# Optimization experiments

Measured on AMD Instinct MI355X. Metric: run time of the kernel, lower is better.

## Reference

```python
import jax, jax.numpy as jnp
import numpy as np

N_NODES = 50000
N_EDGES = 800000
D = 128        # in_channels == out_channels
EDGE_DIM = 32
EPS = 0.0      # GINEConv default eps


def setup_inputs() -> dict:
    key = jax.random.key(0)
    ks = jax.random.split(key, 12)
    s = lambda d: 1.0 / np.sqrt(d)
    inp = {
        "x": jax.random.normal(ks[0], (N_NODES, D), jnp.float32),
        "edge_index": jax.random.randint(ks[1], (2, N_EDGES), 0, N_NODES, jnp.int64),
        "edge_attr": jax.random.normal(ks[2], (N_EDGES, EDGE_DIM), jnp.float32),
        "importance": jax.random.uniform(ks[3], (N_NODES, 1), jnp.float32),
        # GINEConv edge lin: Linear(edge_dim, in_channels)
        "We": jax.random.uniform(ks[4], (EDGE_DIM, D), jnp.float32, -s(EDGE_DIM), s(EDGE_DIM)),
        "be": jax.random.uniform(ks[5], (D,), jnp.float32, -s(EDGE_DIM), s(EDGE_DIM)),
        # GINEConv nn: Linear(in_channels, out_channels)
        "Wc": jax.random.uniform(ks[6], (D, D), jnp.float32, -s(D), s(D)),
        "bc": jax.random.uniform(ks[7], (D,), jnp.float32, -s(D), s(D)),
        # importance_gate: Linear(out_channels + 1, out_channels)
        "Wg": jax.random.uniform(ks[8], (D + 1, D), jnp.float32, -s(D + 1), s(D + 1)),
        "bg": jax.random.uniform(ks[9], (D,), jnp.float32, -s(D + 1), s(D + 1)),
        # importance_propagation: Linear(out_channels, 1)
        "Wp": jax.random.uniform(ks[10], (D, 1), jnp.float32, -s(D), s(D)),
        "bp": jax.random.uniform(ks[11], (1,), jnp.float32, -s(D), s(D)),
    }
    return inp


def reference(x, edge_index, edge_attr, importance, We, be, Wc, bc, Wg, bg, Wp, bp):
    src, dst = edge_index[0], edge_index[1]
    # GINEConv: messages = relu(x_j + lin(edge_attr)), aggregated by sum at dst
    e = edge_attr @ We + be                      # [E, D]
    msg = jax.nn.relu(x[src] + e)                # [E, D] gather + fused add/relu
    agg = jax.ops.segment_sum(msg, dst, num_segments=N_NODES)  # [N, D] scatter-add
    conv_out = ((1.0 + EPS) * x + agg) @ Wc + bc  # [N, D]
    # importance gating + residual
    gate_in = jnp.concatenate([conv_out, importance], axis=-1)  # [N, D+1]
    gate = jax.nn.sigmoid(gate_in @ Wg + bg)
    out = gate * conv_out + (1.0 - gate) * x
    propagated_importance = out @ Wp + bp        # [N, 1]
    return (out, propagated_importance)
```

## Files before the change

### kernel.cpp

```cpp
#include <hip/hip_runtime.h>

#define NN 50000
#define NE 800000
#define DD 128
#define ED 32
#define NB 196

typedef short  bf16x8 __attribute__((ext_vector_type(8)));
typedef float  f32x4  __attribute__((ext_vector_type(4)));
typedef float  f32x16 __attribute__((ext_vector_type(16)));

__device__ __forceinline__ float4 ld4(const float* p) {
    return *reinterpret_cast<const float4*>(p);
}
__device__ __forceinline__ short f2bf(float f) {
    unsigned u = __float_as_uint(f);
    u += 0x7fffu + ((u >> 16) & 1u);
    return (short)(u >> 16);
}
__device__ __forceinline__ float bf2f(short h) {
    return __uint_as_float(((unsigned)(unsigned short)h) << 16);
}
__device__ __forceinline__ int sniff64(const int* ei) {
    return ((ei[1] | ei[3] | ei[5] | ei[7]) == 0) ? 1 : 0;
}

__global__ __launch_bounds__(256)
void k_setup(const float* __restrict__ x, const int* __restrict__ ei,
             const float* __restrict__ We, unsigned int* __restrict__ xb,
             int* __restrict__ counts, unsigned short* __restrict__ Bft)
{
    const int tid = threadIdx.x;
    if (blockIdx.x < 6250) {
        const int t = blockIdx.x * 256 + tid;
        if (t >= NN * 32) return;
        const int n = t >> 5, c = t & 31;
        const float* xr = x + (size_t)n * DD + c;
        const unsigned b0 = (unsigned short)f2bf(xr[0]);
        const unsigned b1 = (unsigned short)f2bf(xr[32]);
        const unsigned b2 = (unsigned short)f2bf(xr[64]);
        const unsigned b3 = (unsigned short)f2bf(xr[96]);
        xb[(size_t)n * 64 + c * 2]     = b0 | (b1 << 16);
        xb[(size_t)n * 64 + c * 2 + 1] = b2 | (b3 << 16);
    } else if (blockIdx.x < 8298) {
        const int is64 = sniff64(ei);
        const int2* ei2 = (const int2*)ei;
        for (int e = (blockIdx.x - 6250) * 256 + tid; e < NE; e += 2048 * 256) {
            const int dst = is64 ? ei2[NE + e].x : ei[NE + e];
            atomicAdd(&counts[dst], 1);
        }
    } else if (tid < 64) {
        const int col = tid & 31, h = tid >> 5;
#pragma unroll
        for (int bb = 0; bb < 4; ++bb)
#pragma unroll
            for (int s = 0; s < 2; ++s)
#pragma unroll
                for (int i = 0; i < 8; ++i)
                    Bft[tid * 64 + (bb * 2 + s) * 8 + i] =
                        (unsigned short)f2bf(We[(s * 16 + h * 8 + i) * DD + bb * 32 + col]);
    }
}

__global__ __launch_bounds__(256)
void k_bsum(const int* __restrict__ counts, int* __restrict__ bsum) {
    const int i = blockIdx.x * 256 + threadIdx.x;
    int c = (i < NN) ? counts[i] : 0;
#pragma unroll
    for (int off = 32; off; off >>= 1) c += __shfl_xor(c, off, 64);
    __shared__ int ws4[4];
    if ((threadIdx.x & 63) == 0) ws4[threadIdx.x >> 6] = c;
    __syncthreads();
    if (threadIdx.x == 0) bsum[blockIdx.x] = ws4[0] + ws4[1] + ws4[2] + ws4[3];
}

__global__ __launch_bounds__(256)
void k_scanb(const int* __restrict__ bsum, int* __restrict__ bexcl) {
    const int tid = threadIdx.x, lane = tid & 63, w = tid >> 6;
    const int v = (tid < NB) ? bsum[tid] : 0;
    int s = v;
#pragma unroll
    for (int off = 1; off < 64; off <<= 1) {
        const int t = __shfl_up(s, off, 64);
        if (lane >= off) s += t;
    }
    __shared__ int wsum[4], wexcl[4];
    if (lane == 63) wsum[w] = s;
    __syncthreads();
    if (tid == 0) {
        int r = 0;
#pragma unroll
        for (int k = 0; k < 4; ++k) { wexcl[k] = r; r += wsum[k]; }
    }
    __syncthreads();
    if (tid < NB) bexcl[tid] = wexcl[w] + s - v;
}

__global__ __launch_bounds__(256)
void k_rowptr(const int* __restrict__ counts, const int* __restrict__ bexcl,
              int* __restrict__ cursor) {
    const int tid = threadIdx.x, lane = tid & 63, w = tid >> 6;
    const int i = blockIdx.x * 256 + tid;
    const int c = (i < NN) ? counts[i] : 0;
    int s = c;
#pragma unroll
    for (int off = 1; off < 64; off <<= 1) {
        const int t = __shfl_up(s, off, 64);
        if (lane >= off) s += t;
    }
    __shared__ int wsum[4], wexcl[4];
    if (lane == 63) wsum[w] = s;
    __syncthreads();
    if (tid == 0) {
        int r = 0;
#pragma unroll
        for (int k = 0; k < 4; ++k) { wexcl[k] = r; r += wsum[k]; }
    }
    __syncthreads();
    if (i < NN) cursor[i] = bexcl[blockIdx.x] + wexcl[w] + s - c;
}

__global__ __launch_bounds__(256)
void k_scatter2(const int* __restrict__ ei, int* __restrict__ cursor,
                const float* __restrict__ ea, int* __restrict__ sdat4,
                unsigned int* __restrict__ ebs)
{
    const int tid = threadIdx.x;
    const int e0  = blockIdx.x * 128;
    __shared__ int spos[128];
    if (tid < 128) {
        const int is64 = sniff64(ei);
        const int2* ei2 = (const int2*)ei;
        const int e   = e0 + tid;
        const int src = is64 ? ei2[e].x : ei[e];
        const int dst = is64 ? ei2[NE + e].x : ei[NE + e];
        const int pos = atomicAdd(&cursor[dst], 1);
        sdat4[pos] = src | (dst << 16);
        spos[tid] = pos;
    }
    __syncthreads();
#pragma unroll
    for (int it = 0; it < 8; ++it) {
        const int task = it * 256 + tid;
        const int el   = task >> 4;
        const int part = task & 15;
        const float2 v = *reinterpret_cast<const float2*>(
                             ea + (size_t)(e0 + el) * ED + part * 2);
        const unsigned lo = (unsigned short)f2bf(v.x);
        const unsigned hi = (unsigned short)f2bf(v.y);
        ebs[(size_t)spos[el] * 16 + part] = lo | (hi << 16);
    }
}

__device__ __forceinline__ void agg_epilogue(f32x16 (&C)[4], const float beb[4],
                                             int dstv, int lane, int col, int h,
                                             float* __restrict__ agg)
{
#pragma unroll
    for (int bb = 0; bb < 4; ++bb)
#pragma unroll
        for (int reg = 0; reg < 16; ++reg)
            C[bb][reg] = fmaxf(C[bb][reg] + beb[bb], 0.0f);

    const int  prv  = __shfl(dstv, (lane == 0) ? 0 : lane - 1, 64);
    const bool flag = (lane < 32) && ((col == 0) || (dstv != prv));
    unsigned rem = (unsigned)(__ballot(flag) & 0xFFFFFFFFull);

    while (rem) {
        const int ms = __ffs((int)rem) - 1;
        rem &= rem - 1;
        const int hi = rem ? (__ffs((int)rem) - 1) : 32;
        const int d  = __shfl(dstv, ms, 64);

        float v0 = 0.f, v1 = 0.f, v2 = 0.f, v3 = 0.f;
#pragma unroll
        for (int reg = 0; reg < 16; ++reg) {
            const int E = (reg & 3) + 8 * (reg >> 2) + 4 * h;
            const float mk = (E >= ms && E < hi) ? 1.0f : 0.0f;
            v0 = fmaf(mk, C[0][reg], v0);
            v1 = fmaf(mk, C[1][reg], v1);
            v2 = fmaf(mk, C[2][reg], v2);
            v3 = fmaf(mk, C[3][reg], v3);
        }
        v0 += __shfl_xor(v0, 32, 64);
        v1 += __shfl_xor(v1, 32, 64);
        v2 += __shfl_xor(v2, 32, 64);
        v3 += __shfl_xor(v3, 32, 64);

        float* ar = agg + (size_t)d * DD + h * 64 + col;
        unsafeAtomicAdd(ar,      h ? v2 : v0);
        unsafeAtomicAdd(ar + 32, h ? v3 : v1);
    }
}

__global__ __launch_bounds__(256, 2)
void k_aggE(const unsigned int* __restrict__ xb, const unsigned int* __restrict__ ebs,
            const unsigned short* __restrict__ Bft, const float* __restrict__ be,
            const int* __restrict__ sdat4, float* __restrict__ agg)
{
    const int lane = threadIdx.x & 63;
    const int col  = lane & 31;
    const int h    = lane >> 5;
    const int wid  = (blockIdx.x << 2) | (threadIdx.x >> 6);
    const int c0   = wid * 2, c1 = wid * 2 + 1;

    bf16x8 Bf[4][2];
    {
        const bf16x8* bp_ = reinterpret_cast<const bf16x8*>(Bft + lane * 64);
#pragma unroll
        for (int bb = 0; bb < 4; ++bb) {
            Bf[bb][0] = bp_[bb * 2];
            Bf[bb][1] = bp_[bb * 2 + 1];
        }
    }
    float beb[4];
#pragma unroll
    for (int bb = 0; bb < 4; ++bb) beb[bb] = be[bb * 32 + col];

    const int sd0 = sdat4[c0 * 32 + col];
    const int sd1 = sdat4[c1 * 32 + col];
    const unsigned int* ebr0 = ebs + ((size_t)c0 * 32 + col) * 16;
    const unsigned int* ebr1 = ebs + ((size_t)c1 * 32 + col) * 16;
    const bf16x8 A00 = *reinterpret_cast<const bf16x8*>(ebr0 + h * 4);
    const bf16x8 A01 = *reinterpret_cast<const bf16x8*>(ebr0 + 8 + h * 4);
    const bf16x8 A10 = *reinterpret_cast<const bf16x8*>(ebr1 + h * 4);
    const bf16x8 A11 = *reinterpret_cast<const bf16x8*>(ebr1 + 8 + h * 4);

    uint2 w0[16];
#pragma unroll
    for (int reg = 0; reg < 16; ++reg) {
        const int E   = (reg & 3) + 8 * (reg >> 2) + 4 * h;
        const int src = __shfl(sd0, E, 64) & 0xFFFF;
        w0[reg] = *reinterpret_cast<const uint2*>(xb + (size_t)src * 64 + col * 2);
    }

    f32x16 C[4];
#pragma unroll
    for (int reg = 0; reg < 16; ++reg) {
        C[0][reg] = __uint_as_float(w0[reg].x << 16);
        C[1][reg] = __uint_as_float(w0[reg].x & 0xFFFF0000u);
        C[2][reg] = __uint_as_float(w0[reg].y << 16);
        C[3][reg] = __uint_as_float(w0[reg].y & 0xFFFF0000u);
    }
#pragma unroll
    for (int bb = 0; bb < 4; ++bb) {
        C[bb] = __builtin_amdgcn_mfma_f32_32x32x16_bf16(A00, Bf[bb][0], C[bb], 0, 0, 0);
        C[bb] = __builtin_amdgcn_mfma_f32_32x32x16_bf16(A01, Bf[bb][1], C[bb], 0, 0, 0);
    }

    uint2 w1[16];
#pragma unroll
    for (int reg = 0; reg < 16; ++reg) {
        const int E   = (reg & 3) + 8 * (reg >> 2) + 4 * h;
        const int src = __shfl(sd1, E, 64) & 0xFFFF;
        w1[reg] = *reinterpret_cast<const uint2*>(xb + (size_t)src * 64 + col * 2);
    }

    agg_epilogue(C, beb, ((unsigned)sd0) >> 16, lane, col, h, agg);

#pragma unroll
    for (int reg = 0; reg < 16; ++reg) {
        C[0][reg] = __uint_as_float(w1[reg].x << 16);
        C[1][reg] = __uint_as_float(w1[reg].x & 0xFFFF0000u);
        C[2][reg] = __uint_as_float(w1[reg].y << 16);
        C[3][reg] = __uint_as_float(w1[reg].y & 0xFFFF0000u);
    }
#pragma unroll
    for (int bb = 0; bb < 4; ++bb) {
        C[bb] = __builtin_amdgcn_mfma_f32_32x32x16_bf16(A10, Bf[bb][0], C[bb], 0, 0, 0);
        C[bb] = __builtin_amdgcn_mfma_f32_32x32x16_bf16(A11, Bf[bb][1], C[bb], 0, 0, 0);
    }
    agg_epilogue(C, beb, ((unsigned)sd1) >> 16, lane, col, h, agg);
}

__global__ __launch_bounds__(256)
void k_cg(const float* __restrict__ x, const float* agg,
          const float* __restrict__ Wc, const float* __restrict__ bc,
          const float* __restrict__ imp, const float* __restrict__ Wg,
          const float* __restrict__ bg, const float* __restrict__ Wp,
          const float* __restrict__ bp, float* outp, float* __restrict__ prop)
{
    __shared__ short sBh[2048 * 8];
    __shared__ short sBl[2048 * 8];
    for (int idx = threadIdx.x; idx < 2048; idx += 256) {
        const int kk = idx >> 9;
        const int b  = (idx >> 6) & 7;
        const int l  = idx & 63;
        const int row0 = kk * 32 + ((l >> 4) << 3);
        const int col  = b * 16 + (l & 15);
        bf16x8 h8, l8;
#pragma unroll
        for (int j = 0; j < 8; ++j) {
            const float v = Wc[(row0 + j) * DD + col];
            const short h = f2bf(v);
            h8[j] = h;
            l8[j] = f2bf(v - bf2f(h));
        }
        *reinterpret_cast<bf16x8*>(&sBh[idx * 8]) = h8;
        *reinterpret_cast<bf16x8*>(&sBl[idx * 8]) = l8;
    }
    __syncthreads();

    const int lane = threadIdx.x & 63;
    const int ncol = lane & 15;
    const int krow = (lane >> 4) << 3;
    const int grp  = lane >> 4;
    const int wib  = threadIdx.x >> 6;
    const int wid  = (blockIdx.x << 2) | wib;
    const bool live = (wid < NN / 16);
    const int m0 = live ? wid * 16 : 0;

    f32x4 C[8];
#pragma unroll
    for (int b = 0; b < 8; ++b) {
        const float bcv = bc[b * 16 + ncol];
        f32x4 c = { bcv, bcv, bcv, bcv };
        C[b] = c;
    }
    {
        const float* xrow = x   + (size_t)(m0 + ncol) * DD + krow;
        const float* grow = agg + (size_t)(m0 + ncol) * DD + krow;
#pragma unroll
        for (int kk = 0; kk < 4; ++kk) {
            const float4 x0 = ld4(xrow + kk * 32), x1 = ld4(xrow + kk * 32 + 4);
            const float4 g0 = ld4(grow + kk * 32), g1 = ld4(grow + kk * 32 + 4);
            const float av[8] = { x0.x + g0.x, x0.y + g0.y, x0.z + g0.z, x0.w + g0.w,
                                  x1.x + g1.x, x1.y + g1.y, x1.z + g1.z, x1.w + g1.w };
            bf16x8 Ah, Al;
#pragma unroll
            for (int j = 0; j < 8; ++j) {
                const short h = f2bf(av[j]);
                Ah[j] = h;
                Al[j] = f2bf(av[j] - bf2f(h));
            }
#pragma unroll
            for (int b = 0; b < 8; ++b) {
                const bf16x8 Bh = *reinterpret_cast<const bf16x8*>(&sBh[((kk * 8 + b) * 64 + lane) * 8]);
                const bf16x8 Bl = *reinterpret_cast<const bf16x8*>(&sBl[((kk * 8 + b) * 64 + lane) * 8]);
                C[b] = __builtin_amdgcn_mfma_f32_16x16x32_bf16(Ah, Bh, C[b], 0, 0, 0);
                C[b] = __builtin_amdgcn_mfma_f32_16x16x32_bf16(Al, Bh, C[b], 0, 0, 0);
                C[b] = __builtin_amdgcn_mfma_f32_16x16x32_bf16(Ah, Bl, C[b], 0, 0, 0);
            }
        }
    }
    __syncthreads();

    for (int idx = threadIdx.x; idx < 2048; idx += 256) {
        const int kk = idx >> 9;
        const int b  = (idx >> 6) & 7;
        const int l  = idx & 63;
        const int row0 = kk * 32 + ((l >> 4) << 3);
        const int col  = b * 16 + (l & 15);
        bf16x8 h8;
#pragma unroll
        for (int j = 0; j < 8; ++j)
            h8[j] = f2bf(Wg[(row0 + j) * DD + col]);
        *reinterpret_cast<bf16x8*>(&sBh[idx * 8]) = h8;
    }
    float* scr = reinterpret_cast<float*>(sBl) + wib * 2048;
#pragma unroll
    for (int r = 0; r < 4; ++r)
#pragma unroll
        for (int b = 0; b < 8; ++b)
            scr[(grp * 4 + r) * DD + b * 16 + ncol] = C[b][r];
    __syncthreads();

    f32x4 Z[8];
#pragma unroll
    for (int b = 0; b < 8; ++b) {
        const float bgv = bg[b * 16 + ncol];
        f32x4 z = { bgv, bgv, bgv, bgv };
        Z[b] = z;
    }
#pragma unroll
    for (int kk = 0; kk < 4; ++kk) {
        const float4 a0 = ld4(scr + ncol * DD + kk * 32 + krow);
        const float4 a1 = ld4(scr + ncol * DD + kk * 32 + krow + 4);
        const float av[8] = { a0.x, a0.y, a0.z, a0.w, a1.x, a1.y, a1.z, a1.w };
        bf16x8 Ah;
#pragma unroll
        for (int j = 0; j < 8; ++j) Ah[j] = f2bf(av[j]);
#pragma unroll
        for (int b = 0; b < 8; ++b) {
            const bf16x8 Bh = *reinterpret_cast<const bf16x8*>(&sBh[((kk * 8 + b) * 64 + lane) * 8]);
            Z[b] = __builtin_amdgcn_mfma_f32_16x16x32_bf16(Ah, Bh, Z[b], 0, 0, 0);
        }
    }

    if (!live) return;

    float wgi[8], wp8[8];
#pragma unroll
    for (int b = 0; b < 8; ++b) {
        wgi[b] = Wg[DD * DD + b * 16 + ncol];
        wp8[b] = Wp[b * 16 + ncol];
    }
    const float bps = bp[0];

    float s[4] = { 0.f, 0.f, 0.f, 0.f };
#pragma unroll
    for (int r = 0; r < 4; ++r) {
        const int m = m0 + grp * 4 + r;
        const float im = imp[m];
        const float* xr = x + (size_t)m * DD + ncol;
        float* orow = outp + (size_t)m * DD + ncol;
#pragma unroll
        for (int b = 0; b < 8; ++b) {
            const float a = Z[b][r] + im * wgi[b];
            const float g = 1.0f / (1.0f + expf(-a));
            const float xv = xr[b * 16];
            const float o = fmaf(g, C[b][r] - xv, xv);
            orow[b * 16] = o;
            s[r] += o * wp8[b];
        }
    }
#pragma unroll
    for (int off = 1; off < 16; off <<= 1) {
        s[0] += __shfl_xor(s[0], off, 64);
        s[1] += __shfl_xor(s[1], off, 64);
        s[2] += __shfl_xor(s[2], off, 64);
        s[3] += __shfl_xor(s[3], off, 64);
    }
    if (ncol < 4) {
        const float v = (ncol == 0) ? s[0] : (ncol == 1) ? s[1] : (ncol == 2) ? s[2] : s[3];
        prop[m0 + grp * 4 + ncol] = v + bps;
    }
}

extern "C" void kernel_launch(void* const* d_in, const int* in_sizes, int n_in,
                              void* d_out, int out_size, void* d_ws, size_t ws_size,
                              hipStream_t stream) {
    const float* x   = (const float*)d_in[0];
    const int*   ei  = (const int*)d_in[1];
    const float* ea  = (const float*)d_in[2];
    const float* imp = (const float*)d_in[3];
    const float* We  = (const float*)d_in[4];
    const float* be  = (const float*)d_in[5];
    const float* Wc  = (const float*)d_in[6];
    const float* bc  = (const float*)d_in[7];
    const float* Wg  = (const float*)d_in[8];
    const float* bg  = (const float*)d_in[9];
    const float* Wp  = (const float*)d_in[10];
    const float* bp  = (const float*)d_in[11];

    float* out  = (float*)d_out;
    float* prop = out + (size_t)NN * DD;
    float* agg  = out;

    int*            counts = (int*)d_ws;
    int*            cursor = (int*)((char*)d_ws + 204800);
    int*            bsum   = (int*)((char*)d_ws + 409600);
    int*            bexcl  = (int*)((char*)d_ws + 413696);
    unsigned short* Bft    = (unsigned short*)((char*)d_ws + 417792);
    int*            sdat4  = (int*)((char*)d_ws + 1048576);
    unsigned int*   xb     = (unsigned int*)((char*)d_ws + 4456448);
    unsigned int*   ebs    = (unsigned int*)((char*)d_ws + 17301504);

    hipMemsetAsync(counts, 0, NN * sizeof(int), stream);
    hipMemsetAsync(agg, 0, (size_t)NN * DD * sizeof(float), stream);
    hipLaunchKernelGGL(k_setup,    dim3(8299), dim3(256), 0, stream,
                       x, ei, We, xb, counts, Bft);
    hipLaunchKernelGGL(k_bsum,     dim3(NB),   dim3(256), 0, stream, counts, bsum);
    hipLaunchKernelGGL(k_scanb,    dim3(1),    dim3(256), 0, stream, bsum, bexcl);
    hipLaunchKernelGGL(k_rowptr,   dim3(NB),   dim3(256), 0, stream, counts, bexcl, cursor);
    hipLaunchKernelGGL(k_scatter2, dim3(6250), dim3(256), 0, stream, ei, cursor, ea, sdat4, ebs);
    hipLaunchKernelGGL(k_aggE,     dim3(3125), dim3(256), 0, stream,
                       xb, ebs, Bft, be, sdat4, agg);
    hipLaunchKernelGGL(k_cg,       dim3(782),  dim3(256), 0, stream,
                       x, agg, Wc, bc, imp, Wg, bg, Wp, bp, out, prop);
}
```

Before: 207.1 us.

## Gather edge_attr directly in aggregation instead of pre-permuting bf16 copy

The scatter kernel no longer writes a bf16 copy of edge_attr reordered by destination. It now stores an (src|dst, original edge id) pair per sorted slot, and the aggregation kernel gathers fp32 edge_attr rows by edge id and converts them to bf16 in registers. This removes one full read-convert-write pass over the edge features, about 51 MB of fp32 read plus a bf16 write. The cost is that the aggregation kernel now does random 128-byte row gathers of fp32 data (twice the bytes of the bf16 copy), plus extra conversion ALU work and a wider per-edge index.

```diff
diff --git a/kernel.cpp b/kernel.cpp
--- a/kernel.cpp
+++ b/kernel.cpp
@@ -121,34 +121,16 @@
 }
 
 __global__ __launch_bounds__(256)
-void k_scatter2(const int* __restrict__ ei, int* __restrict__ cursor,
-                const float* __restrict__ ea, int* __restrict__ sdat4,
-                unsigned int* __restrict__ ebs)
-{
-    const int tid = threadIdx.x;
-    const int e0  = blockIdx.x * 128;
-    __shared__ int spos[128];
-    if (tid < 128) {
-        const int is64 = sniff64(ei);
-        const int2* ei2 = (const int2*)ei;
-        const int e   = e0 + tid;
+void k_scatter(const int* __restrict__ ei, int* __restrict__ cursor,
+               int2* __restrict__ sdat) {
+    const int is64 = sniff64(ei);
+    const int2* ei2 = (const int2*)ei;
+    for (int e = blockIdx.x * blockDim.x + threadIdx.x; e < NE;
+         e += gridDim.x * blockDim.x) {
         const int src = is64 ? ei2[e].x : ei[e];
         const int dst = is64 ? ei2[NE + e].x : ei[NE + e];
         const int pos = atomicAdd(&cursor[dst], 1);
-        sdat4[pos] = src | (dst << 16);
-        spos[tid] = pos;
-    }
-    __syncthreads();
-#pragma unroll
-    for (int it = 0; it < 8; ++it) {
-        const int task = it * 256 + tid;
-        const int el   = task >> 4;
-        const int part = task & 15;
-        const float2 v = *reinterpret_cast<const float2*>(
-                             ea + (size_t)(e0 + el) * ED + part * 2);
-        const unsigned lo = (unsigned short)f2bf(v.x);
-        const unsigned hi = (unsigned short)f2bf(v.y);
-        ebs[(size_t)spos[el] * 16 + part] = lo | (hi << 16);
+        sdat[pos] = make_int2(src | (dst << 16), e);
     }
 }
 
@@ -194,9 +176,9 @@
 }
 
 __global__ __launch_bounds__(256, 2)
-void k_aggE(const unsigned int* __restrict__ xb, const unsigned int* __restrict__ ebs,
+void k_aggE(const unsigned int* __restrict__ xb, const float* __restrict__ ea,
             const unsigned short* __restrict__ Bft, const float* __restrict__ be,
-            const int* __restrict__ sdat4, float* __restrict__ agg)
+            const int2* __restrict__ sdat, float* __restrict__ agg)
 {
     const int lane = threadIdx.x & 63;
     const int col  = lane & 31;
@@ -217,22 +199,26 @@
 #pragma unroll
     for (int bb = 0; bb < 4; ++bb) beb[bb] = be[bb * 32 + col];
 
-    const int sd0 = sdat4[c0 * 32 + col];
-    const int sd1 = sdat4[c1 * 32 + col];
-    const unsigned int* ebr0 = ebs + ((size_t)c0 * 32 + col) * 16;
-    const unsigned int* ebr1 = ebs + ((size_t)c1 * 32 + col) * 16;
-    const bf16x8 A00 = *reinterpret_cast<const bf16x8*>(ebr0 + h * 4);
-    const bf16x8 A01 = *reinterpret_cast<const bf16x8*>(ebr0 + 8 + h * 4);
-    const bf16x8 A10 = *reinterpret_cast<const bf16x8*>(ebr1 + h * 4);
-    const bf16x8 A11 = *reinterpret_cast<const bf16x8*>(ebr1 + 8 + h * 4);
+    const int2 dv0 = sdat[(size_t)c0 * 32 + col];
+    const int2 dv1 = sdat[(size_t)c1 * 32 + col];
+
+    const float* ear0 = ea + (size_t)dv0.y * ED + h * 8;
+    const float4 e00 = ld4(ear0),      e01 = ld4(ear0 + 4);
+    const float4 e02 = ld4(ear0 + 16), e03 = ld4(ear0 + 20);
 
     uint2 w0[16];
 #pragma unroll
     for (int reg = 0; reg < 16; ++reg) {
         const int E   = (reg & 3) + 8 * (reg >> 2) + 4 * h;
-        const int src = __shfl(sd0, E, 64) & 0xFFFF;
+        const int src = __shfl(dv0.x, E, 64) & 0xFFFF;
         w0[reg] = *reinterpret_cast<const uint2*>(xb + (size_t)src * 64 + col * 2);
     }
+
+    bf16x8 Af0, Af1;
+    Af0[0] = f2bf(e00.x); Af0[1] = f2bf(e00.y); Af0[2] = f2bf(e00.z); Af0[3] = f2bf(e00.w);
+    Af0[4] = f2bf(e01.x); Af0[5] = f2bf(e01.y); Af0[6] = f2bf(e01.z); Af0[7] = f2bf(e01.w);
+    Af1[0] = f2bf(e02.x); Af1[1] = f2bf(e02.y); Af1[2] = f2bf(e02.z); Af1[3] = f2bf(e02.w);
+    Af1[4] = f2bf(e03.x); Af1[5] = f2bf(e03.y); Af1[6] = f2bf(e03.z); Af1[7] = f2bf(e03.w);
 
     f32x16 C[4];
 #pragma unroll
@@ -244,19 +230,27 @@
     }
 #pragma unroll
     for (int bb = 0; bb < 4; ++bb) {
-        C[bb] = __builtin_amdgcn_mfma_f32_32x32x16_bf16(A00, Bf[bb][0], C[bb], 0, 0, 0);
-        C[bb] = __builtin_amdgcn_mfma_f32_32x32x16_bf16(A01, Bf[bb][1], C[bb], 0, 0, 0);
-    }
-
+        C[bb] = __builtin_amdgcn_mfma_f32_32x32x16_bf16(Af0, Bf[bb][0], C[bb], 0, 0, 0);
+        C[bb] = __builtin_amdgcn_mfma_f32_32x32x16_bf16(Af1, Bf[bb][1], C[bb], 0, 0, 0);
+    }
+
+    const float* ear1 = ea + (size_t)dv1.y * ED + h * 8;
+    const float4 e10 = ld4(ear1),      e11 = ld4(ear1 + 4);
+    const float4 e12 = ld4(ear1 + 16), e13 = ld4(ear1 + 20);
     uint2 w1[16];
 #pragma unroll
     for (int reg = 0; reg < 16; ++reg) {
         const int E   = (reg & 3) + 8 * (reg >> 2) + 4 * h;
-        const int src = __shfl(sd1, E, 64) & 0xFFFF;
+        const int src = __shfl(dv1.x, E, 64) & 0xFFFF;
         w1[reg] = *reinterpret_cast<const uint2*>(xb + (size_t)src * 64 + col * 2);
     }
 
-    agg_epilogue(C, beb, ((unsigned)sd0) >> 16, lane, col, h, agg);
+    agg_epilogue(C, beb, ((unsigned)dv0.x) >> 16, lane, col, h, agg);
+
+    Af0[0] = f2bf(e10.x); Af0[1] = f2bf(e10.y); Af0[2] = f2bf(e10.z); Af0[3] = f2bf(e10.w);
+    Af0[4] = f2bf(e11.x); Af0[5] = f2bf(e11.y); Af0[6] = f2bf(e11.z); Af0[7] = f2bf(e11.w);
+    Af1[0] = f2bf(e12.x); Af1[1] = f2bf(e12.y); Af1[2] = f2bf(e12.z); Af1[3] = f2bf(e12.w);
+    Af1[4] = f2bf(e13.x); Af1[5] = f2bf(e13.y); Af1[6] = f2bf(e13.z); Af1[7] = f2bf(e13.w);
 
 #pragma unroll
     for (int reg = 0; reg < 16; ++reg) {
@@ -267,10 +261,10 @@
     }
 #pragma unroll
     for (int bb = 0; bb < 4; ++bb) {
-        C[bb] = __builtin_amdgcn_mfma_f32_32x32x16_bf16(A10, Bf[bb][0], C[bb], 0, 0, 0);
-        C[bb] = __builtin_amdgcn_mfma_f32_32x32x16_bf16(A11, Bf[bb][1], C[bb], 0, 0, 0);
-    }
-    agg_epilogue(C, beb, ((unsigned)sd1) >> 16, lane, col, h, agg);
+        C[bb] = __builtin_amdgcn_mfma_f32_32x32x16_bf16(Af0, Bf[bb][0], C[bb], 0, 0, 0);
+        C[bb] = __builtin_amdgcn_mfma_f32_32x32x16_bf16(Af1, Bf[bb][1], C[bb], 0, 0, 0);
+    }
+    agg_epilogue(C, beb, ((unsigned)dv1.x) >> 16, lane, col, h, agg);
 }
 
 __global__ __launch_bounds__(256)
@@ -452,20 +446,19 @@
     int*            bsum   = (int*)((char*)d_ws + 409600);
     int*            bexcl  = (int*)((char*)d_ws + 413696);
     unsigned short* Bft    = (unsigned short*)((char*)d_ws + 417792);
-    int*            sdat4  = (int*)((char*)d_ws + 1048576);
-    unsigned int*   xb     = (unsigned int*)((char*)d_ws + 4456448);
-    unsigned int*   ebs    = (unsigned int*)((char*)d_ws + 17301504);
+    int2*           sdat   = (int2*)((char*)d_ws + 1048576);
+    unsigned int*   xb     = (unsigned int*)((char*)d_ws + 7448576);
 
     hipMemsetAsync(counts, 0, NN * sizeof(int), stream);
     hipMemsetAsync(agg, 0, (size_t)NN * DD * sizeof(float), stream);
-    hipLaunchKernelGGL(k_setup,    dim3(8299), dim3(256), 0, stream,
+    hipLaunchKernelGGL(k_setup,   dim3(8299), dim3(256), 0, stream,
                        x, ei, We, xb, counts, Bft);
-    hipLaunchKernelGGL(k_bsum,     dim3(NB),   dim3(256), 0, stream, counts, bsum);
-    hipLaunchKernelGGL(k_scanb,    dim3(1),    dim3(256), 0, stream, bsum, bexcl);
-    hipLaunchKernelGGL(k_rowptr,   dim3(NB),   dim3(256), 0, stream, counts, bexcl, cursor);
-    hipLaunchKernelGGL(k_scatter2, dim3(6250), dim3(256), 0, stream, ei, cursor, ea, sdat4, ebs);
-    hipLaunchKernelGGL(k_aggE,     dim3(3125), dim3(256), 0, stream,
-                       xb, ebs, Bft, be, sdat4, agg);
-    hipLaunchKernelGGL(k_cg,       dim3(782),  dim3(256), 0, stream,
+    hipLaunchKernelGGL(k_bsum,    dim3(NB),   dim3(256), 0, stream, counts, bsum);
+    hipLaunchKernelGGL(k_scanb,   dim3(1),    dim3(256), 0, stream, bsum, bexcl);
+    hipLaunchKernelGGL(k_rowptr,  dim3(NB),   dim3(256), 0, stream, counts, bexcl, cursor);
+    hipLaunchKernelGGL(k_scatter, dim3(2048), dim3(256), 0, stream, ei, cursor, sdat);
+    hipLaunchKernelGGL(k_aggE,    dim3(3125), dim3(256), 0, stream,
+                       xb, ea, Bft, be, sdat, agg);
+    hipLaunchKernelGGL(k_cg,      dim3(782),  dim3(256), 0, stream,
                        x, agg, Wc, bc, imp, Wg, bg, Wp, bp, out, prop);
 }
```

Result: slower. 218.5 us (+5.5%).
